# Kernel tuning notes

Measured on AMD Instinct MI355X. Metric: run time of the kernel, lower is better.

## Reference

```python
import jax, jax.numpy as jnp
from jax import lax
import numpy as np

B, CIN, COUT, H, W = 32, 64, 64, 128, 128
KH = KW = 1
STRIDE = (1, 1)
PADDING = ((0, 0), (0, 0))


def setup_inputs() -> dict:
    key = jax.random.key(0)
    k1, k2, k3, k4 = jax.random.split(key, 4)
    x_quant = jax.random.randint(k1, (B, CIN, H, W), 0, 256, dtype=jnp.int32)  # uint8 values
    weight_int8 = jax.random.randint(k2, (COUT, CIN, KH, KW), -127, 128, dtype=jnp.int32)
    weight_scale = jax.random.uniform(k3, (COUT, 1, 1, 1), dtype=jnp.float32, minval=0.001, maxval=0.02)
    weight_zero_point = jnp.zeros((COUT, 1, 1, 1), dtype=jnp.int32)
    bias_fp32 = jax.random.normal(k4, (COUT,), dtype=jnp.float32) * 0.1
    return {
        "x_quant": x_quant,
        "input_scale": jnp.float32(0.02),
        "input_zero_point": jnp.int32(128),
        "weight_int8": weight_int8,
        "weight_scale": weight_scale,
        "weight_zero_point": weight_zero_point,
        "bias_fp32": bias_fp32,
        "output_scale": jnp.float32(0.05),
        "output_zero_point": jnp.int32(128),
    }


def reference(x_quant, input_scale, input_zero_point, weight_int8, weight_scale,
              weight_zero_point, bias_fp32, output_scale, output_zero_point):
    # dequant (zero-point subtract) in fp32
    x = x_quant.astype(jnp.float32) - input_zero_point.astype(jnp.float32)          # [B,Cin,H,W]
    w = weight_int8.astype(jnp.float32) - weight_zero_point.astype(jnp.float32)     # [O,I,kh,kw]
    conv = lax.conv_general_dilated(
        x, w, window_strides=STRIDE, padding=PADDING,
        dimension_numbers=("NCHW", "OIHW", "NCHW"))                                 # [B,O,H',W']
    # requantize: per-out-channel scale + bias, round, clamp to uint8 range
    requant_scale = (input_scale * weight_scale / output_scale).reshape(1, COUT, 1, 1)
    bias_term = (bias_fp32 / output_scale).reshape(1, COUT, 1, 1)
    final_float = conv * requant_scale + bias_term
    requant = jnp.round(final_float) + output_zero_point.astype(jnp.float32)
    out_q = jnp.clip(requant, 0.0, 255.0).astype(jnp.uint8)
    return out_q
```

## Files before the change

kernel.cpp:

```cpp
#include <hip/hip_runtime.h>

#define CIN   64
#define COUT  64
#define HW    16384
#define NPIX  (32 * HW)

__global__ void prep_kernel(const int* __restrict__ w,
                            const float* __restrict__ wscale,
                            const int* __restrict__ wzp,
                            const float* __restrict__ bias,
                            const float* __restrict__ is_p,
                            const float* __restrict__ os_p,
                            const int* __restrict__ ozp_p,
                            int* __restrict__ wp,
                            float4* __restrict__ params) {
    int o = threadIdx.x;
    if (o >= COUT) return;
    int zp = wzp[o];
    int sum = 0;
    #pragma unroll
    for (int k = 0; k < 16; ++k) {
        int c0 = w[o * CIN + 4 * k + 0] - zp;
        int c1 = w[o * CIN + 4 * k + 1] - zp;
        int c2 = w[o * CIN + 4 * k + 2] - zp;
        int c3 = w[o * CIN + 4 * k + 3] - zp;
        sum += c0 + c1 + c2 + c3;
        wp[o * 16 + k] = (c0 & 0xff) | ((c1 & 0xff) << 8) |
                         ((c2 & 0xff) << 16) | ((c3 & 0xff) << 24);
    }
    float scale = is_p[0] * wscale[o] / os_p[0];
    float bterm = bias[o] / os_p[0] + (float)ozp_p[0];
    float4 pr;
    pr.x = scale;
    pr.y = bterm;
    pr.z = __int_as_float(sum);
    pr.w = 0.0f;
    params[o] = pr;
}

__global__ __launch_bounds__(256) void conv_kernel(
    const int* __restrict__ x,
    const int* __restrict__ wp_g,
    const float4* __restrict__ params_g,
    const int* __restrict__ izp_p,
    int* __restrict__ out) {

    __shared__ int4  s_wp[COUT * 4];
    __shared__ float4 s_par[COUT];

    int tid = threadIdx.x;
    s_wp[tid] = ((const int4*)wp_g)[tid];
    if (tid < COUT) s_par[tid] = params_g[tid];
    int izp_adj = izp_p[0] - 128;
    __syncthreads();

    int t = blockIdx.x * 256 + tid;
    int b = t >> 14;
    int p = t & (HW - 1);

    const int* xb = x + b * (CIN * HW) + p;

    int px[16];
    #pragma unroll
    for (int cg = 0; cg < 16; ++cg) {
        int v0 = xb[(4 * cg + 0) * HW];
        int v1 = xb[(4 * cg + 1) * HW];
        int v2 = xb[(4 * cg + 2) * HW];
        int v3 = xb[(4 * cg + 3) * HW];
        px[cg] = (v0 | (v1 << 8) | (v2 << 16) | (v3 << 24)) ^ 0x80808080;
    }

    int* ob = out + b * (COUT * HW) + p;

    #pragma unroll 8
    for (int o = 0; o < COUT; ++o) {
        int4 w0 = s_wp[o * 4 + 0];
        int4 w1 = s_wp[o * 4 + 1];
        int4 w2 = s_wp[o * 4 + 2];
        int4 w3 = s_wp[o * 4 + 3];
        float4 pr = s_par[o];
        int wsum = __float_as_int(pr.z);
        int acc = -izp_adj * wsum;

        acc = __builtin_amdgcn_sdot4(px[0],  w0.x, acc, false);
        acc = __builtin_amdgcn_sdot4(px[1],  w0.y, acc, false);
        acc = __builtin_amdgcn_sdot4(px[2],  w0.z, acc, false);
        acc = __builtin_amdgcn_sdot4(px[3],  w0.w, acc, false);
        acc = __builtin_amdgcn_sdot4(px[4],  w1.x, acc, false);
        acc = __builtin_amdgcn_sdot4(px[5],  w1.y, acc, false);
        acc = __builtin_amdgcn_sdot4(px[6],  w1.z, acc, false);
        acc = __builtin_amdgcn_sdot4(px[7],  w1.w, acc, false);
        acc = __builtin_amdgcn_sdot4(px[8],  w2.x, acc, false);
        acc = __builtin_amdgcn_sdot4(px[9],  w2.y, acc, false);
        acc = __builtin_amdgcn_sdot4(px[10], w2.z, acc, false);
        acc = __builtin_amdgcn_sdot4(px[11], w2.w, acc, false);
        acc = __builtin_amdgcn_sdot4(px[12], w3.x, acc, false);
        acc = __builtin_amdgcn_sdot4(px[13], w3.y, acc, false);
        acc = __builtin_amdgcn_sdot4(px[14], w3.z, acc, false);
        acc = __builtin_amdgcn_sdot4(px[15], w3.w, acc, false);

        float f = fmaf((float)acc, pr.x, pr.y);
        f = rintf(f);
        f = fminf(fmaxf(f, 0.0f), 255.0f);
        __builtin_nontemporal_store((int)f, ob + o * HW);
    }
}

extern "C" void kernel_launch(void* const* d_in, const int* in_sizes, int n_in,
                              void* d_out, int out_size, void* d_ws, size_t ws_size,
                              hipStream_t stream) {
    const int*   x      = (const int*)d_in[0];
    const float* is_p   = (const float*)d_in[1];
    const int*   izp_p  = (const int*)d_in[2];
    const int*   w      = (const int*)d_in[3];
    const float* wscale = (const float*)d_in[4];
    const int*   wzp    = (const int*)d_in[5];
    const float* bias   = (const float*)d_in[6];
    const float* os_p   = (const float*)d_in[7];
    const int*   ozp_p  = (const int*)d_in[8];

    int* out = (int*)d_out;

    int*    wp     = (int*)d_ws;
    float4* params = (float4*)((char*)d_ws + 4096);

    prep_kernel<<<1, 64, 0, stream>>>(w, wscale, wzp, bias, is_p, os_p, ozp_p, wp, params);

    conv_kernel<<<2048, 256, 0, stream>>>(x, wp, params, izp_p, out);
}
```

Baseline: 253.3 us.

## Process two pixels per thread, prefetching the second pixel's inputs during the first's compute

Each thread now handles two pixels, one from each half of the pixel range, with half as many blocks. While the first pixel's 64 output channels are computed, the second pixel's 64 channel loads are issued in staggered groups of four and packed. The aim is to hide global load latency behind the dot-product work. The input zero-point correction is also folded into a precomputed per-channel accumulator init in the prep kernel. The change raises register pressure and halves the grid, which may reduce occupancy.

Result: slower. 285.4 us (+12.7%).

```diff
diff --git a/kernel.cpp b/kernel.cpp
--- a/kernel.cpp
+++ b/kernel.cpp
@@ -4,12 +4,14 @@
 #define COUT  64
 #define HW    16384
 #define NPIX  (32 * HW)
+#define HALF  (NPIX / 2)
 
 __global__ void prep_kernel(const int* __restrict__ w,
                             const float* __restrict__ wscale,
                             const int* __restrict__ wzp,
                             const float* __restrict__ bias,
                             const float* __restrict__ is_p,
+                            const int* __restrict__ izp_p,
                             const float* __restrict__ os_p,
                             const int* __restrict__ ozp_p,
                             int* __restrict__ wp,
@@ -28,82 +30,111 @@
         wp[o * 16 + k] = (c0 & 0xff) | ((c1 & 0xff) << 8) |
                          ((c2 & 0xff) << 16) | ((c3 & 0xff) << 24);
     }
-    float scale = is_p[0] * wscale[o] / os_p[0];
-    float bterm = bias[o] / os_p[0] + (float)ozp_p[0];
     float4 pr;
-    pr.x = scale;
-    pr.y = bterm;
-    pr.z = __int_as_float(sum);
-    pr.w = 0.0f;
+    pr.x = is_p[0] * wscale[o] / os_p[0];
+    pr.y = bias[o] / os_p[0] + (float)ozp_p[0];
+    pr.z = 0.0f;
+    pr.w = __int_as_float((128 - izp_p[0]) * sum);
     params[o] = pr;
+}
+
+__device__ __forceinline__ int pack4(int v0, int v1, int v2, int v3) {
+    return (v0 | (v1 << 8) | (v2 << 16) | (v3 << 24)) ^ 0x80808080;
+}
+
+template <bool PREF>
+__device__ __forceinline__ void pixel_pass(const int* __restrict__ s_wp,
+                                           const float4* __restrict__ s_par,
+                                           const int px[16], int nx[16],
+                                           const int* __restrict__ xn,
+                                           int* __restrict__ ob) {
+    int buf[4][4];
+    if constexpr (PREF) {
+        #pragma unroll
+        for (int d = 0; d < 4; ++d) {
+            buf[d][0] = xn[(4 * d + 0) * HW];
+            buf[d][1] = xn[(4 * d + 1) * HW];
+            buf[d][2] = xn[(4 * d + 2) * HW];
+            buf[d][3] = xn[(4 * d + 3) * HW];
+        }
+    }
+    #pragma unroll
+    for (int c = 0; c < 16; ++c) {
+        #pragma unroll
+        for (int oo = 0; oo < 4; ++oo) {
+            int o = c * 4 + oo;
+            const int4* wv = (const int4*)(s_wp + o * 16);
+            int4 w0 = wv[0], w1 = wv[1], w2 = wv[2], w3 = wv[3];
+            float4 pr = s_par[o];
+            int acc = __float_as_int(pr.w);
+
+            acc = __builtin_amdgcn_sdot4(px[0],  w0.x, acc, false);
+            acc = __builtin_amdgcn_sdot4(px[1],  w0.y, acc, false);
+            acc = __builtin_amdgcn_sdot4(px[2],  w0.z, acc, false);
+            acc = __builtin_amdgcn_sdot4(px[3],  w0.w, acc, false);
+            acc = __builtin_amdgcn_sdot4(px[4],  w1.x, acc, false);
+            acc = __builtin_amdgcn_sdot4(px[5],  w1.y, acc, false);
+            acc = __builtin_amdgcn_sdot4(px[6],  w1.z, acc, false);
+            acc = __builtin_amdgcn_sdot4(px[7],  w1.w, acc, false);
+            acc = __builtin_amdgcn_sdot4(px[8],  w2.x, acc, false);
+            acc = __builtin_amdgcn_sdot4(px[9],  w2.y, acc, false);
+            acc = __builtin_amdgcn_sdot4(px[10], w2.z, acc, false);
+            acc = __builtin_amdgcn_sdot4(px[11], w2.w, acc, false);
+            acc = __builtin_amdgcn_sdot4(px[12], w3.x, acc, false);
+            acc = __builtin_amdgcn_sdot4(px[13], w3.y, acc, false);
+            acc = __builtin_amdgcn_sdot4(px[14], w3.z, acc, false);
+            acc = __builtin_amdgcn_sdot4(px[15], w3.w, acc, false);
+
+            float f = fmaf((float)acc, pr.x, pr.y);
+            f = rintf(f);
+            f = fminf(fmaxf(f, 0.0f), 255.0f);
+            __builtin_nontemporal_store((int)f, ob + o * HW);
+        }
+        if constexpr (PREF) {
+            nx[c] = pack4(buf[c & 3][0], buf[c & 3][1], buf[c & 3][2], buf[c & 3][3]);
+            if (c < 12) {
+                int cg = c + 4;
+                buf[c & 3][0] = xn[(4 * cg + 0) * HW];
+                buf[c & 3][1] = xn[(4 * cg + 1) * HW];
+                buf[c & 3][2] = xn[(4 * cg + 2) * HW];
+                buf[c & 3][3] = xn[(4 * cg + 3) * HW];
+            }
+        }
+    }
 }
 
 __global__ __launch_bounds__(256) void conv_kernel(
     const int* __restrict__ x,
     const int* __restrict__ wp_g,
     const float4* __restrict__ params_g,
-    const int* __restrict__ izp_p,
     int* __restrict__ out) {
 
-    __shared__ int4  s_wp[COUT * 4];
+    __shared__ int    s_wp[COUT * 16];
     __shared__ float4 s_par[COUT];
 
     int tid = threadIdx.x;
-    s_wp[tid] = ((const int4*)wp_g)[tid];
+    ((int4*)s_wp)[tid] = ((const int4*)wp_g)[tid];
     if (tid < COUT) s_par[tid] = params_g[tid];
-    int izp_adj = izp_p[0] - 128;
     __syncthreads();
 
-    int t = blockIdx.x * 256 + tid;
-    int b = t >> 14;
-    int p = t & (HW - 1);
+    int t  = blockIdx.x * 256 + tid;
+    int tB = t + HALF;
+    int bA = t  >> 14, pA = t  & (HW - 1);
+    int bB = tB >> 14, pB = tB & (HW - 1);
 
-    const int* xb = x + b * (CIN * HW) + p;
+    const int* xA = x + bA * (CIN * HW) + pA;
+    const int* xB = x + bB * (CIN * HW) + pB;
+    int* obA = out + bA * (COUT * HW) + pA;
+    int* obB = out + bB * (COUT * HW) + pB;
 
-    int px[16];
+    int px[16], nx[16];
     #pragma unroll
-    for (int cg = 0; cg < 16; ++cg) {
-        int v0 = xb[(4 * cg + 0) * HW];
-        int v1 = xb[(4 * cg + 1) * HW];
-        int v2 = xb[(4 * cg + 2) * HW];
-        int v3 = xb[(4 * cg + 3) * HW];
-        px[cg] = (v0 | (v1 << 8) | (v2 << 16) | (v3 << 24)) ^ 0x80808080;
-    }
+    for (int cg = 0; cg < 16; ++cg)
+        px[cg] = pack4(xA[(4 * cg + 0) * HW], xA[(4 * cg + 1) * HW],
+                       xA[(4 * cg + 2) * HW], xA[(4 * cg + 3) * HW]);
 
-    int* ob = out + b * (COUT * HW) + p;
-
-    #pragma unroll 8
-    for (int o = 0; o < COUT; ++o) {
-        int4 w0 = s_wp[o * 4 + 0];
-        int4 w1 = s_wp[o * 4 + 1];
-        int4 w2 = s_wp[o * 4 + 2];
-        int4 w3 = s_wp[o * 4 + 3];
-        float4 pr = s_par[o];
-        int wsum = __float_as_int(pr.z);
-        int acc = -izp_adj * wsum;
-
-        acc = __builtin_amdgcn_sdot4(px[0],  w0.x, acc, false);
-        acc = __builtin_amdgcn_sdot4(px[1],  w0.y, acc, false);
-        acc = __builtin_amdgcn_sdot4(px[2],  w0.z, acc, false);
-        acc = __builtin_amdgcn_sdot4(px[3],  w0.w, acc, false);
-        acc = __builtin_amdgcn_sdot4(px[4],  w1.x, acc, false);
-        acc = __builtin_amdgcn_sdot4(px[5],  w1.y, acc, false);
-        acc = __builtin_amdgcn_sdot4(px[6],  w1.z, acc, false);
-        acc = __builtin_amdgcn_sdot4(px[7],  w1.w, acc, false);
-        acc = __builtin_amdgcn_sdot4(px[8],  w2.x, acc, false);
-        acc = __builtin_amdgcn_sdot4(px[9],  w2.y, acc, false);
-        acc = __builtin_amdgcn_sdot4(px[10], w2.z, acc, false);
-        acc = __builtin_amdgcn_sdot4(px[11], w2.w, acc, false);
-        acc = __builtin_amdgcn_sdot4(px[12], w3.x, acc, false);
-        acc = __builtin_amdgcn_sdot4(px[13], w3.y, acc, false);
-        acc = __builtin_amdgcn_sdot4(px[14], w3.z, acc, false);
-        acc = __builtin_amdgcn_sdot4(px[15], w3.w, acc, false);
-
-        float f = fmaf((float)acc, pr.x, pr.y);
-        f = rintf(f);
-        f = fminf(fmaxf(f, 0.0f), 255.0f);
-        __builtin_nontemporal_store((int)f, ob + o * HW);
-    }
+    pixel_pass<true >(s_wp, s_par, px, nx, xB, obA);
+    pixel_pass<false>(s_wp, s_par, nx, px, xB, obB);
 }
 
 extern "C" void kernel_launch(void* const* d_in, const int* in_sizes, int n_in,
@@ -124,7 +155,8 @@
     int*    wp     = (int*)d_ws;
     float4* params = (float4*)((char*)d_ws + 4096);
 
-    prep_kernel<<<1, 64, 0, stream>>>(w, wscale, wzp, bias, is_p, os_p, ozp_p, wp, params);
+    prep_kernel<<<1, 64, 0, stream>>>(w, wscale, wzp, bias, is_p, izp_p, os_p,
+                                      ozp_p, wp, params);
 
-    conv_kernel<<<2048, 256, 0, stream>>>(x, wp, params, izp_p, out);
+    conv_kernel<<<1024, 256, 0, stream>>>(x, wp, params, out);
 }
```

## Double-buffer input tiles via global_load_lds and split output channels across half-blocks

Applied to the files above, without the earlier changes.

The conv kernel becomes persistent-style: 512 blocks each process 1024 pixels in groups of 128. Input channels are prefetched into double-buffered LDS with async global_load_lds while the previous group is computed. Each half of the block computes 32 of the 64 output channels for the same 128 pixels, reading weights and params straight from global/scalar memory instead of LDS. The zero-point correction is folded into prep, removing a kernel argument. This trades launch parallelism (fewer blocks) and per-thread work for overlap of loads with compute, and adds LDS bank traffic when unpacking.

Result: slower. 276.8 us (+9.3%).

```diff
diff --git a/kernel.cpp b/kernel.cpp
--- a/kernel.cpp
+++ b/kernel.cpp
@@ -5,11 +5,17 @@
 #define HW    16384
 #define NPIX  (32 * HW)
 
+#define BLOCKS 512
+#define SPAN   1024
+#define GRP    128
+#define NGRP   (SPAN / GRP)
+
 __global__ void prep_kernel(const int* __restrict__ w,
                             const float* __restrict__ wscale,
                             const int* __restrict__ wzp,
                             const float* __restrict__ bias,
                             const float* __restrict__ is_p,
+                            const int* __restrict__ izp_p,
                             const float* __restrict__ os_p,
                             const int* __restrict__ ozp_p,
                             int* __restrict__ wp,
@@ -28,13 +34,11 @@
         wp[o * 16 + k] = (c0 & 0xff) | ((c1 & 0xff) << 8) |
                          ((c2 & 0xff) << 16) | ((c3 & 0xff) << 24);
     }
-    float scale = is_p[0] * wscale[o] / os_p[0];
-    float bterm = bias[o] / os_p[0] + (float)ozp_p[0];
     float4 pr;
-    pr.x = scale;
-    pr.y = bterm;
-    pr.z = __int_as_float(sum);
-    pr.w = 0.0f;
+    pr.x = is_p[0] * wscale[o] / os_p[0];
+    pr.y = bias[o] / os_p[0] + (float)ozp_p[0];
+    pr.z = 0.0f;
+    pr.w = __int_as_float((128 - izp_p[0]) * sum);
     params[o] = pr;
 }
 
@@ -42,67 +46,83 @@
     const int* __restrict__ x,
     const int* __restrict__ wp_g,
     const float4* __restrict__ params_g,
-    const int* __restrict__ izp_p,
     int* __restrict__ out) {
 
-    __shared__ int4  s_wp[COUT * 4];
-    __shared__ float4 s_par[COUT];
+    __shared__ int s_x[2][CIN * GRP];
 
-    int tid = threadIdx.x;
-    s_wp[tid] = ((const int4*)wp_g)[tid];
-    if (tid < COUT) s_par[tid] = params_g[tid];
-    int izp_adj = izp_p[0] - 128;
-    __syncthreads();
+    const int tid  = threadIdx.x;
+    const int lane = tid & 63;
+    const int wv   = tid >> 6;
+    const int px   = tid & (GRP - 1);
+    const int oh   = __builtin_amdgcn_readfirstlane(tid >> 7);
 
-    int t = blockIdx.x * 256 + tid;
-    int b = t >> 14;
-    int p = t & (HW - 1);
+    const int pix_base = blockIdx.x * SPAN;
+    const int bimg = pix_base >> 14;
+    const int p0   = pix_base & (HW - 1);
+    const int* ximg = x   + bimg * (CIN * HW) + p0;
+    int*       oimg = out + bimg * (COUT * HW) + p0;
 
-    const int* xb = x + b * (CIN * HW) + p;
+    auto issue = [&](int g, int nb) {
+        const int* gbase = ximg + g * GRP + ((lane & 31) * 4);
+        #pragma unroll
+        for (int j = 0; j < 8; ++j) {
+            int c = wv * 16 + 2 * j + (lane >> 5);
+            const int* gp = gbase + c * HW;
+            int* lp = &s_x[nb][(wv * 16 + 2 * j) * GRP];
+            __builtin_amdgcn_global_load_lds(
+                (const __attribute__((address_space(1))) void*)gp,
+                (__attribute__((address_space(3))) void*)lp, 16, 0, 0);
+        }
+    };
 
-    int px[16];
-    #pragma unroll
-    for (int cg = 0; cg < 16; ++cg) {
-        int v0 = xb[(4 * cg + 0) * HW];
-        int v1 = xb[(4 * cg + 1) * HW];
-        int v2 = xb[(4 * cg + 2) * HW];
-        int v3 = xb[(4 * cg + 3) * HW];
-        px[cg] = (v0 | (v1 << 8) | (v2 << 16) | (v3 << 24)) ^ 0x80808080;
-    }
+    issue(0, 0);
 
-    int* ob = out + b * (COUT * HW) + p;
+    for (int g = 0; g < NGRP; ++g) {
+        __syncthreads();
+        if (g + 1 < NGRP) issue(g + 1, (g + 1) & 1);
 
-    #pragma unroll 8
-    for (int o = 0; o < COUT; ++o) {
-        int4 w0 = s_wp[o * 4 + 0];
-        int4 w1 = s_wp[o * 4 + 1];
-        int4 w2 = s_wp[o * 4 + 2];
-        int4 w3 = s_wp[o * 4 + 3];
-        float4 pr = s_par[o];
-        int wsum = __float_as_int(pr.z);
-        int acc = -izp_adj * wsum;
+        const int* xp = &s_x[g & 1][px];
+        int pk[16];
+        #pragma unroll
+        for (int cg = 0; cg < 16; ++cg) {
+            int v0 = xp[(4 * cg + 0) * GRP];
+            int v1 = xp[(4 * cg + 1) * GRP];
+            int v2 = xp[(4 * cg + 2) * GRP];
+            int v3 = xp[(4 * cg + 3) * GRP];
+            pk[cg] = (v0 | (v1 << 8) | (v2 << 16) | (v3 << 24)) ^ 0x80808080;
+        }
 
-        acc = __builtin_amdgcn_sdot4(px[0],  w0.x, acc, false);
-        acc = __builtin_amdgcn_sdot4(px[1],  w0.y, acc, false);
-        acc = __builtin_amdgcn_sdot4(px[2],  w0.z, acc, false);
-        acc = __builtin_amdgcn_sdot4(px[3],  w0.w, acc, false);
-        acc = __builtin_amdgcn_sdot4(px[4],  w1.x, acc, false);
-        acc = __builtin_amdgcn_sdot4(px[5],  w1.y, acc, false);
-        acc = __builtin_amdgcn_sdot4(px[6],  w1.z, acc, false);
-        acc = __builtin_amdgcn_sdot4(px[7],  w1.w, acc, false);
-        acc = __builtin_amdgcn_sdot4(px[8],  w2.x, acc, false);
-        acc = __builtin_amdgcn_sdot4(px[9],  w2.y, acc, false);
-        acc = __builtin_amdgcn_sdot4(px[10], w2.z, acc, false);
-        acc = __builtin_amdgcn_sdot4(px[11], w2.w, acc, false);
-        acc = __builtin_amdgcn_sdot4(px[12], w3.x, acc, false);
-        acc = __builtin_amdgcn_sdot4(px[13], w3.y, acc, false);
-        acc = __builtin_amdgcn_sdot4(px[14], w3.z, acc, false);
-        acc = __builtin_amdgcn_sdot4(px[15], w3.w, acc, false);
+        int* og = oimg + g * GRP + px;
+        #pragma unroll 4
+        for (int i = 0; i < 32; ++i) {
+            int o = oh * 32 + i;
+            const int4* wvp = (const int4*)(wp_g + o * 16);
+            int4 w0 = wvp[0], w1 = wvp[1], w2 = wvp[2], w3 = wvp[3];
+            float4 pr = params_g[o];
+            int acc = __float_as_int(pr.w);
 
-        float f = fmaf((float)acc, pr.x, pr.y);
-        f = rintf(f);
-        f = fminf(fmaxf(f, 0.0f), 255.0f);
-        __builtin_nontemporal_store((int)f, ob + o * HW);
+            acc = __builtin_amdgcn_sdot4(pk[0],  w0.x, acc, false);
+            acc = __builtin_amdgcn_sdot4(pk[1],  w0.y, acc, false);
+            acc = __builtin_amdgcn_sdot4(pk[2],  w0.z, acc, false);
+            acc = __builtin_amdgcn_sdot4(pk[3],  w0.w, acc, false);
+            acc = __builtin_amdgcn_sdot4(pk[4],  w1.x, acc, false);
+            acc = __builtin_amdgcn_sdot4(pk[5],  w1.y, acc, false);
+            acc = __builtin_amdgcn_sdot4(pk[6],  w1.z, acc, false);
+            acc = __builtin_amdgcn_sdot4(pk[7],  w1.w, acc, false);
+            acc = __builtin_amdgcn_sdot4(pk[8],  w2.x, acc, false);
+            acc = __builtin_amdgcn_sdot4(pk[9],  w2.y, acc, false);
+            acc = __builtin_amdgcn_sdot4(pk[10], w2.z, acc, false);
+            acc = __builtin_amdgcn_sdot4(pk[11], w2.w, acc, false);
+            acc = __builtin_amdgcn_sdot4(pk[12], w3.x, acc, false);
+            acc = __builtin_amdgcn_sdot4(pk[13], w3.y, acc, false);
+            acc = __builtin_amdgcn_sdot4(pk[14], w3.z, acc, false);
+            acc = __builtin_amdgcn_sdot4(pk[15], w3.w, acc, false);
+
+            float f = fmaf((float)acc, pr.x, pr.y);
+            f = rintf(f);
+            f = fminf(fmaxf(f, 0.0f), 255.0f);
+            __builtin_nontemporal_store((int)f, og + o * HW);
+        }
     }
 }
 
@@ -124,7 +144,8 @@
     int*    wp     = (int*)d_ws;
     float4* params = (float4*)((char*)d_ws + 4096);
 
-    prep_kernel<<<1, 64, 0, stream>>>(w, wscale, wzp, bias, is_p, os_p, ozp_p, wp, params);
+    prep_kernel<<<1, 64, 0, stream>>>(w, wscale, wzp, bias, is_p, izp_p, os_p,
+                                      ozp_p, wp, params);
 
-    conv_kernel<<<2048, 256, 0, stream>>>(x, wp, params, izp_p, out);
+    conv_kernel<<<BLOCKS, 256, 0, stream>>>(x, wp, params, out);
 }
```
